# Kernel optimization log

Hardware: AMD Instinct MI355X
Metric: run time of the kernel (lower is better)

Reference implementation:

```python
import jax, jax.numpy as jnp
import numpy as np

N_NODES = 100000
MAX_DEG = 128
BATCH = 16384
NUM_SAMPLES = 25


def setup_inputs() -> dict:
    key = jax.random.key(0)
    k1, k2, k3 = jax.random.split(key, 3)
    adj_weight = jax.random.uniform(k1, (N_NODES, MAX_DEG), dtype=jnp.float32)
    adj_info = jax.random.randint(k2, (N_NODES, MAX_DEG), 0, N_NODES, dtype=jnp.int32)
    ids = jax.random.randint(k3, (BATCH,), 0, N_NODES, dtype=jnp.int64)
    return {
        "adj_weight": adj_weight,
        "adj_info": adj_info,
        "ids": ids,
        "num_samples": NUM_SAMPLES,
    }


def reference(adj_weight, adj_info, ids, num_samples):
    # Gather per-node neighbor lists and weights: [B, max_deg]
    adj_lists = adj_info[ids]
    adj_weight_lists = adj_weight[ids]
    # tf.multinomial(tf.log(w), num_samples): categorical sampling with
    # replacement, probabilities proportional to weights.
    logits = jnp.log(adj_weight_lists)  # [B, max_deg]
    skey = jax.random.key(42)
    # categorical over last axis; draw num_samples per row -> [B, num_samples]
    idx = jax.random.categorical(
        skey, logits, axis=-1, shape=(num_samples, ids.shape[0])
    ).T
    # Gather sampled neighbor ids (equivalent to the flattened bias+gather trick)
    res = jnp.take_along_axis(adj_lists, idx, axis=1)  # [B, num_samples]
    return res
```

## Files before the change

kernel.cpp:

```cpp
#include <hip/hip_runtime.h>
#include <stdint.h>


#define MAXDEG 128

__device__ __forceinline__ uint32_t rotl32(uint32_t x, int r) {
  return __builtin_rotateleft32(x, r);
}

__device__ __forceinline__ uint32_t tf_bits(uint32_t i) {
  uint32_t x0, x1;
  x1 = i + 42u; x0 = x1;
  x1 = rotl32(x1, 13) ^ x0;
  x0 += x1; x1 = rotl32(x1, 15) ^ x0;
  x0 += x1; x1 = rotl32(x1, 26) ^ x0;
  x0 += x1; x1 = rotl32(x1,  6) ^ x0;
  x1 += 0x1BD11BF1u; x0 = x0 + x1 + 42u;
  x1 = rotl32(x1, 17) ^ x0;
  x0 += x1; x1 = rotl32(x1, 29) ^ x0;
  x0 += x1; x1 = rotl32(x1, 16) ^ x0;
  x0 += x1; x1 = rotl32(x1, 24) ^ x0;
  x1 += 2u; x0 = x0 + x1 + 0x1BD11BF0u;
  x1 = rotl32(x1, 13) ^ x0;
  x0 += x1; x1 = rotl32(x1, 15) ^ x0;
  x0 += x1; x1 = rotl32(x1, 26) ^ x0;
  x0 += x1; x1 = rotl32(x1,  6) ^ x0;
  x1 += 45u; x0 = x0 + x1;
  x1 = rotl32(x1, 17) ^ x0;
  x0 += x1; x1 = rotl32(x1, 29) ^ x0;
  x0 += x1; x1 = rotl32(x1, 16) ^ x0;
  x0 += x1; x1 = rotl32(x1, 24) ^ x0;
  x1 += 0x1BD11BF4u; x0 = x0 + x1 + 42u;
  x1 = rotl32(x1, 13) ^ x0;
  x0 += x1; x1 = rotl32(x1, 15) ^ x0;
  x0 += x1; x1 = rotl32(x1, 26) ^ x0;
  x0 += x1; x1 = rotl32(x1,  6) ^ x0;
  return (x0 + 0x1BD11BF0u) ^ (x1 + 5u);
}

__device__ __forceinline__ float uniform_from_bits(uint32_t bits) {
  uint32_t fb = (bits >> 9) | 0x3f800000u;
  float f = __uint_as_float(fb) - 1.0f;
  return fmaxf(f, 1.17549435e-38f);
}

__device__ __forceinline__ float zscore(float lwp, uint32_t bits) {
  const float l = __log2f(uniform_from_bits(bits));
  const float t = __log2f(-l);
  return __builtin_fmaf(-0.69314718056f, t, lwp);
}

template <int CTRL>
__device__ __forceinline__ float dpp_max_step(float z) {
  const int t = __builtin_amdgcn_update_dpp(0, __float_as_int(z), CTRL, 0xF, 0xF, true);
  return fmaxf(z, __int_as_float(t));
}

__device__ __forceinline__ float swz_max16(float z) {
  return fmaxf(z, __int_as_float(
      __builtin_amdgcn_ds_swizzle(__float_as_int(z), 0x401F)));
}

__device__ __attribute__((noinline)) int resolve_f64(
    float4 wv, uint32_t sbase, int l) {
  const uint32_t bits0 = tf_bits(sbase + 0u);
  const uint32_t bits1 = tf_bits(sbase + 1u);
  const uint32_t bits2 = tf_bits(sbase + 2u);
  const uint32_t bits3 = tf_bits(sbase + 3u);
  double bz = log((double)wv.x) - log(-log((double)uniform_from_bits(bits0)));
  int bd = 4 * l;
  const double Z1 = log((double)wv.y) - log(-log((double)uniform_from_bits(bits1)));
  if (Z1 > bz) { bz = Z1; bd = 4 * l + 1; }
  const double Z2 = log((double)wv.z) - log(-log((double)uniform_from_bits(bits2)));
  if (Z2 > bz) { bz = Z2; bd = 4 * l + 2; }
  const double Z3 = log((double)wv.w) - log(-log((double)uniform_from_bits(bits3)));
  if (Z3 > bz) { bz = Z3; bd = 4 * l + 3; }
  #pragma unroll
  for (int m = 1; m < 32; m <<= 1) {
    const double oz = __shfl_xor(bz, m);
    const int od = __shfl_xor(bd, m);
    if (oz > bz || (oz == bz && od < bd)) { bz = oz; bd = od; }
  }
  return bd;
}

__global__ __launch_bounds__(1024) void wns_kernel(
    const float* __restrict__ adj_weight,
    const int* __restrict__ adj_info,
    const int* __restrict__ ids,
    int* __restrict__ out,
    int batch, int nsamp) {
  const int lane = threadIdx.x & 63;
  const int l = lane & 31;
  const int wid = blockIdx.x * 16 + (threadIdx.x >> 6);
  if (2 * wid >= batch) return;
  const int b = 2 * wid + (lane >> 5);

  const int nid = ids[b];
  const float4 wv = *(const float4*)(adj_weight + nid * MAXDEG + 4 * l);
  const float lwp0 = __logf(wv.x) + 0.36651292f;
  const float lwp1 = __logf(wv.y) + 0.36651292f;
  const float lwp2 = __logf(wv.z) + 0.36651292f;
  const float lwp3 = __logf(wv.w) + 0.36651292f;

  uint32_t sbase = (uint32_t)b * 128u + (uint32_t)(4 * l);
  const uint32_t sstep = (uint32_t)batch * 128u;

  uint32_t flagA = 0u, flagB = 0u;
  int dAcc = 0;

  #pragma unroll 1
  for (int s = 0; s < nsamp; ++s, sbase += sstep) {
    const uint32_t bits0 = tf_bits(sbase + 0u);
    const uint32_t bits1 = tf_bits(sbase + 1u);
    const uint32_t bits2 = tf_bits(sbase + 2u);
    const uint32_t bits3 = tf_bits(sbase + 3u);

    const float z0 = zscore(lwp0, bits0);
    const float z1 = zscore(lwp1, bits1);
    const float z2 = zscore(lwp2, bits2);
    const float z3 = zscore(lwp3, bits3);

    float zmax = fmaxf(fmaxf(fmaxf(z0, z1), z2), z3);
    zmax = dpp_max_step<0x121>(zmax);
    zmax = dpp_max_step<0x122>(zmax);
    zmax = dpp_max_step<0x124>(zmax);
    zmax = dpp_max_step<0x128>(zmax);
    zmax = swz_max16(zmax);

    const float thr = zmax - 3.0e-4f;
    const unsigned long long m0 = __ballot(z0 > thr);
    const unsigned long long m1 = __ballot(z1 > thr);
    const unsigned long long m2 = __ballot(z2 > thr);
    const unsigned long long m3 = __ballot(z3 > thr);
    const uint32_t a0 = (uint32_t)m0, a1 = (uint32_t)m1,
                   a2 = (uint32_t)m2, a3 = (uint32_t)m3;
    const uint32_t c0 = (uint32_t)(m0 >> 32), c1 = (uint32_t)(m1 >> 32),
                   c2 = (uint32_t)(m2 >> 32), c3 = (uint32_t)(m3 >> 32);
    const int cntA = __popc(a0) + __popc(a1) + __popc(a2) + __popc(a3);
    const int cntB = __popc(c0) + __popc(c1) + __popc(c2) + __popc(c3);

    const int dA = a0 ? 4 * __builtin_ctz(a0)
                 : a1 ? 4 * __builtin_ctz(a1) + 1
                 : a2 ? 4 * __builtin_ctz(a2) + 2
                 : a3 ? 4 * __builtin_ctz(a3) + 3 : 0;
    const int dB = c0 ? 4 * __builtin_ctz(c0)
                 : c1 ? 4 * __builtin_ctz(c1) + 1
                 : c2 ? 4 * __builtin_ctz(c2) + 2
                 : c3 ? 4 * __builtin_ctz(c3) + 3 : 0;
    const int dSel = (lane < 32) ? dA : dB;
    dAcc = ((lane & 31) == s) ? dSel : dAcc;

    flagA |= (cntA != 1) ? (1u << s) : 0u;
    flagB |= (cntB != 1) ? (1u << s) : 0u;
  }

  const uint32_t rowbase = (uint32_t)b * 128u + (uint32_t)(4 * l);
  for (uint32_t m = flagA | flagB; m; m &= m - 1u) {
    const int s = __builtin_ctz(m);
    const int bd = resolve_f64(wv, rowbase + (uint32_t)s * sstep, l);
    const int bdA = __shfl(bd, 0);
    const int bdB = __shfl(bd, 32);
    if (((flagA >> s) & 1u) && lane == s) dAcc = bdA;
    if (((flagB >> s) & 1u) && lane == s + 32) dAcc = bdB;
  }

  if (l < nsamp) {
    out[b * nsamp + l] = adj_info[nid * MAXDEG + dAcc];
  }
}

extern "C" void kernel_launch(void* const* d_in, const int* in_sizes, int n_in,
                              void* d_out, int out_size, void* d_ws, size_t ws_size,
                              hipStream_t stream) {
  const float* adj_weight = (const float*)d_in[0];
  const int* adj_info = (const int*)d_in[1];
  const int* ids = (const int*)d_in[2];
  int batch = in_sizes[2];
  int nsamp = out_size / batch;
  int waves = (batch + 1) / 2;
  int blocks = (waves + 15) / 16;
  wns_kernel<<<blocks, 1024, 0, stream>>>(adj_weight, adj_info, ids,
                                          (int*)d_out, batch, nsamp);
}
```

Baseline: 144.9 us.

## Split sample loop across waves in chunks of five samples

```diff
diff --git a/kernel.cpp b/kernel.cpp
--- a/kernel.cpp
+++ b/kernel.cpp
@@ -3,6 +3,7 @@
 
 
 #define MAXDEG 128
+#define NSCHUNK 5
 
 __device__ __forceinline__ uint32_t rotl32(uint32_t x, int r) {
   return __builtin_rotateleft32(x, r);
@@ -84,7 +85,7 @@
   return bd;
 }
 
-__global__ __launch_bounds__(1024) void wns_kernel(
+__global__ __launch_bounds__(256) void wns_kernel(
     const float* __restrict__ adj_weight,
     const int* __restrict__ adj_info,
     const int* __restrict__ ids,
@@ -92,9 +93,14 @@
     int batch, int nsamp) {
   const int lane = threadIdx.x & 63;
   const int l = lane & 31;
-  const int wid = blockIdx.x * 16 + (threadIdx.x >> 6);
-  if (2 * wid >= batch) return;
-  const int b = 2 * wid + (lane >> 5);
+  const int nchunk = (nsamp + NSCHUNK - 1) / NSCHUNK;
+  const int gw = blockIdx.x * 4 + (threadIdx.x >> 6);
+  const int pair = gw / nchunk;
+  const int chunk = gw - pair * nchunk;
+  if (2 * pair >= batch) return;
+  const int b = 2 * pair + (lane >> 5);
+  const int s0 = chunk * NSCHUNK;
+  const int scnt = min(NSCHUNK, nsamp - s0);
 
   const int nid = ids[b];
   const float4 wv = *(const float4*)(adj_weight + nid * MAXDEG + 4 * l);
@@ -103,14 +109,15 @@
   const float lwp2 = __logf(wv.z) + 0.36651292f;
   const float lwp3 = __logf(wv.w) + 0.36651292f;
 
-  uint32_t sbase = (uint32_t)b * 128u + (uint32_t)(4 * l);
   const uint32_t sstep = (uint32_t)batch * 128u;
+  uint32_t sbase = ((uint32_t)s0 * (uint32_t)batch + (uint32_t)b) * 128u
+                   + (uint32_t)(4 * l);
 
   uint32_t flagA = 0u, flagB = 0u;
   int dAcc = 0;
 
   #pragma unroll 1
-  for (int s = 0; s < nsamp; ++s, sbase += sstep) {
+  for (int k = 0; k < scnt; ++k, sbase += sstep) {
     const uint32_t bits0 = tf_bits(sbase + 0u);
     const uint32_t bits1 = tf_bits(sbase + 1u);
     const uint32_t bits2 = tf_bits(sbase + 2u);
@@ -149,24 +156,25 @@
                  : c2 ? 4 * __builtin_ctz(c2) + 2
                  : c3 ? 4 * __builtin_ctz(c3) + 3 : 0;
     const int dSel = (lane < 32) ? dA : dB;
-    dAcc = ((lane & 31) == s) ? dSel : dAcc;
+    dAcc = ((lane & 31) == k) ? dSel : dAcc;
 
-    flagA |= (cntA != 1) ? (1u << s) : 0u;
-    flagB |= (cntB != 1) ? (1u << s) : 0u;
+    flagA |= (cntA != 1) ? (1u << k) : 0u;
+    flagB |= (cntB != 1) ? (1u << k) : 0u;
   }
 
-  const uint32_t rowbase = (uint32_t)b * 128u + (uint32_t)(4 * l);
+  const uint32_t rowbase = ((uint32_t)s0 * (uint32_t)batch + (uint32_t)b) * 128u
+                           + (uint32_t)(4 * l);
   for (uint32_t m = flagA | flagB; m; m &= m - 1u) {
-    const int s = __builtin_ctz(m);
-    const int bd = resolve_f64(wv, rowbase + (uint32_t)s * sstep, l);
+    const int k = __builtin_ctz(m);
+    const int bd = resolve_f64(wv, rowbase + (uint32_t)k * sstep, l);
     const int bdA = __shfl(bd, 0);
     const int bdB = __shfl(bd, 32);
-    if (((flagA >> s) & 1u) && lane == s) dAcc = bdA;
-    if (((flagB >> s) & 1u) && lane == s + 32) dAcc = bdB;
+    if (((flagA >> k) & 1u) && lane == k) dAcc = bdA;
+    if (((flagB >> k) & 1u) && lane == k + 32) dAcc = bdB;
   }
 
-  if (l < nsamp) {
-    out[b * nsamp + l] = adj_info[nid * MAXDEG + dAcc];
+  if (l < scnt) {
+    out[b * nsamp + s0 + l] = adj_info[nid * MAXDEG + dAcc];
   }
 }
 
@@ -178,8 +186,9 @@
   const int* ids = (const int*)d_in[2];
   int batch = in_sizes[2];
   int nsamp = out_size / batch;
-  int waves = (batch + 1) / 2;
-  int blocks = (waves + 15) / 16;
-  wns_kernel<<<blocks, 1024, 0, stream>>>(adj_weight, adj_info, ids,
-                                          (int*)d_out, batch, nsamp);
+  int nchunk = (nsamp + NSCHUNK - 1) / NSCHUNK;
+  long long waves = (long long)((batch + 1) / 2) * nchunk;
+  int blocks = (int)((waves + 3) / 4);
+  wns_kernel<<<blocks, 256, 0, stream>>>(adj_weight, adj_info, ids,
+                                         (int*)d_out, batch, nsamp);
 }
```

Result: no change. 146.3 us (+1.0%).
